# Optimization experiments

Hardware: AMD Instinct MI355X
Metric: run time of the kernel (lower is better)

The kernel has to match this reference:

```python
import jax, jax.numpy as jnp
import numpy as np

B, D, L = 16384, 4096, 6


def setup_inputs() -> dict:
    key = jax.random.key(0)
    k_x, k_w = jax.random.split(key)
    inputs = jax.random.normal(k_x, (B, D), dtype=jnp.float32)
    # xavier_uniform for each [D, 1] slice: bound = sqrt(6 / (D + 1))
    bound = float(np.sqrt(6.0 / (D + 1)))
    w = jax.random.uniform(k_w, (L, D, 1), dtype=jnp.float32, minval=-bound, maxval=bound)
    b = jnp.zeros((L, D), dtype=jnp.float32)
    return {"inputs": inputs, "w": w, "b": b}


def reference(inputs, w, b):
    # DCN cross layers: x_{i+1} = x0 * (x @ w_i) + b_i + x
    x0 = inputs  # [B, D]

    def step(x, wb):
        wi, bi = wb                      # wi: [D, 1], bi: [D]
        xw = jnp.matmul(x, wi)           # [B, 1] matvec
        x_new = x0 * xw + bi + x         # fused elementwise mul + bias + residual
        return x_new, None

    x, _ = jax.lax.scan(step, inputs, (w, b))
    # use_bn=False, dropout=0 -> output is x
    return x
```

## Files before the change

kernel.cpp:

```cpp
#include <hip/hip_runtime.h>


#define BATCH 16384
#define DIM   4096
#define NLAYER 6
#define BLK 256
#define VPT 4

__global__ __launch_bounds__(BLK) void crossnet_kernel(
    const float* __restrict__ xin,
    const float* __restrict__ w,
    const float* __restrict__ bias,
    float* __restrict__ out)
{
    const int row  = blockIdx.x;
    const int tid  = threadIdx.x;
    const int lane = tid & 63;
    const int wave = tid >> 6;

    const float4* xrow = (const float4*)(xin + (size_t)row * DIM);

    float4 x0v[VPT], xv[VPT];
#pragma unroll
    for (int j = 0; j < VPT; ++j) {
        x0v[j] = xrow[tid + j * BLK];
        xv[j]  = x0v[j];
    }

    __shared__ float red[2][4];

    for (int l = 0; l < NLAYER; ++l) {
        const float4* wl = (const float4*)(w + l * DIM);
        float p = 0.0f;
#pragma unroll
        for (int j = 0; j < VPT; ++j) {
            float4 wv = wl[tid + j * BLK];
            p = fmaf(xv[j].x, wv.x, p);
            p = fmaf(xv[j].y, wv.y, p);
            p = fmaf(xv[j].z, wv.z, p);
            p = fmaf(xv[j].w, wv.w, p);
        }
#pragma unroll
        for (int off = 32; off > 0; off >>= 1)
            p += __shfl_down(p, off, 64);
        if (lane == 0) red[l & 1][wave] = p;
        __syncthreads();
        const float s = red[l & 1][0] + red[l & 1][1] + red[l & 1][2] + red[l & 1][3];

        const float4* bl = (const float4*)(bias + l * DIM);
#pragma unroll
        for (int j = 0; j < VPT; ++j) {
            float4 bv = bl[tid + j * BLK];
            xv[j].x = fmaf(x0v[j].x, s, bv.x + xv[j].x);
            xv[j].y = fmaf(x0v[j].y, s, bv.y + xv[j].y);
            xv[j].z = fmaf(x0v[j].z, s, bv.z + xv[j].z);
            xv[j].w = fmaf(x0v[j].w, s, bv.w + xv[j].w);
        }
    }

    float4* orow = (float4*)(out + (size_t)row * DIM);
#pragma unroll
    for (int j = 0; j < VPT; ++j)
        orow[tid + j * BLK] = xv[j];
}

extern "C" void kernel_launch(void* const* d_in, const int* in_sizes, int n_in,
                              void* d_out, int out_size, void* d_ws, size_t ws_size,
                              hipStream_t stream) {
    const float* xin  = (const float*)d_in[0];
    const float* w    = (const float*)d_in[1];
    const float* bias = (const float*)d_in[2];
    float* out = (float*)d_out;

    crossnet_kernel<<<BATCH, BLK, 0, stream>>>(xin, w, bias, out);
}
```

Measured before the change: 506.5 us.

## Collapse cross layers into one row scale plus a precomputed bias vector

Uses the fact that every layer's state can be written as a_l*x0 + c_l, where a_l is a per-row scalar and c_l is a running sum of biases. The six per-layer dot products x0·w_l are computed together with a single reduction and one barrier. The final row is then formed as a*x0 + c in one pass. A small single-block kernel precomputes c and the scalars c_l·w_l, which adds a launch and a dependency ahead of the main kernel. Floating-point summation order changes.

New measurement: 503.9 us. No clear change (-0.5%).

```diff
diff --git a/kernel.cpp b/kernel.cpp
--- a/kernel.cpp
+++ b/kernel.cpp
@@ -1,16 +1,62 @@
 #include <hip/hip_runtime.h>
 
 
-#define BATCH 16384
-#define DIM   4096
+#define BATCH  16384
+#define DIM    4096
 #define NLAYER 6
-#define BLK 256
-#define VPT 4
+#define BLK    256
+#define VPT    4
+
+__global__ __launch_bounds__(1024) void precompute_kernel(
+    const float* __restrict__ w,
+    const float* __restrict__ bias,
+    float* __restrict__ c_out,
+    float* __restrict__ d_out)
+{
+    const int tid  = threadIdx.x;
+    const int lane = tid & 63;
+    const int wave = tid >> 6;
+
+    float dpart[NLAYER];
+#pragma unroll
+    for (int l = 0; l < NLAYER; ++l) dpart[l] = 0.0f;
+
+#pragma unroll
+    for (int k = 0; k < DIM / 1024; ++k) {
+        const int j = tid + k * 1024;
+        float pre = 0.0f;
+#pragma unroll
+        for (int l = 0; l < NLAYER; ++l) {
+            dpart[l] = fmaf(pre, w[l * DIM + j], dpart[l]);
+            pre += bias[l * DIM + j];
+        }
+        c_out[j] = pre;
+    }
+
+#pragma unroll
+    for (int l = 0; l < NLAYER; ++l)
+#pragma unroll
+        for (int off = 32; off > 0; off >>= 1)
+            dpart[l] += __shfl_xor(dpart[l], off, 64);
+
+    __shared__ float red[16][NLAYER];
+    if (lane == 0)
+#pragma unroll
+        for (int l = 0; l < NLAYER; ++l) red[wave][l] = dpart[l];
+    __syncthreads();
+    if (tid < NLAYER) {
+        float s = 0.0f;
+#pragma unroll
+        for (int wv = 0; wv < 16; ++wv) s += red[wv][tid];
+        d_out[tid] = s;
+    }
+}
 
 __global__ __launch_bounds__(BLK) void crossnet_kernel(
     const float* __restrict__ xin,
     const float* __restrict__ w,
-    const float* __restrict__ bias,
+    const float* __restrict__ c,
+    const float* __restrict__ d,
     float* __restrict__ out)
 {
     const int row  = blockIdx.x;
@@ -20,48 +66,58 @@
 
     const float4* xrow = (const float4*)(xin + (size_t)row * DIM);
 
-    float4 x0v[VPT], xv[VPT];
+    float4 x0v[VPT];
 #pragma unroll
-    for (int j = 0; j < VPT; ++j) {
+    for (int j = 0; j < VPT; ++j)
         x0v[j] = xrow[tid + j * BLK];
-        xv[j]  = x0v[j];
-    }
 
-    __shared__ float red[2][4];
-
+    float u[NLAYER];
+#pragma unroll
+    for (int l = 0; l < NLAYER; ++l) u[l] = 0.0f;
+#pragma unroll
     for (int l = 0; l < NLAYER; ++l) {
         const float4* wl = (const float4*)(w + l * DIM);
-        float p = 0.0f;
 #pragma unroll
         for (int j = 0; j < VPT; ++j) {
             float4 wv = wl[tid + j * BLK];
-            p = fmaf(xv[j].x, wv.x, p);
-            p = fmaf(xv[j].y, wv.y, p);
-            p = fmaf(xv[j].z, wv.z, p);
-            p = fmaf(xv[j].w, wv.w, p);
-        }
-#pragma unroll
-        for (int off = 32; off > 0; off >>= 1)
-            p += __shfl_down(p, off, 64);
-        if (lane == 0) red[l & 1][wave] = p;
-        __syncthreads();
-        const float s = red[l & 1][0] + red[l & 1][1] + red[l & 1][2] + red[l & 1][3];
-
-        const float4* bl = (const float4*)(bias + l * DIM);
-#pragma unroll
-        for (int j = 0; j < VPT; ++j) {
-            float4 bv = bl[tid + j * BLK];
-            xv[j].x = fmaf(x0v[j].x, s, bv.x + xv[j].x);
-            xv[j].y = fmaf(x0v[j].y, s, bv.y + xv[j].y);
-            xv[j].z = fmaf(x0v[j].z, s, bv.z + xv[j].z);
-            xv[j].w = fmaf(x0v[j].w, s, bv.w + xv[j].w);
+            u[l] = fmaf(x0v[j].x, wv.x, u[l]);
+            u[l] = fmaf(x0v[j].y, wv.y, u[l]);
+            u[l] = fmaf(x0v[j].z, wv.z, u[l]);
+            u[l] = fmaf(x0v[j].w, wv.w, u[l]);
         }
     }
 
-    float4* orow = (float4*)(out + (size_t)row * DIM);
 #pragma unroll
-    for (int j = 0; j < VPT; ++j)
-        orow[tid + j * BLK] = xv[j];
+    for (int l = 0; l < NLAYER; ++l)
+#pragma unroll
+        for (int off = 32; off > 0; off >>= 1)
+            u[l] += __shfl_xor(u[l], off, 64);
+
+    __shared__ float red[4][NLAYER];
+    if (lane == 0)
+#pragma unroll
+        for (int l = 0; l < NLAYER; ++l) red[wave][l] = u[l];
+    __syncthreads();
+
+    float a = 1.0f;
+#pragma unroll
+    for (int l = 0; l < NLAYER; ++l) {
+        const float s = red[0][l] + red[1][l] + red[2][l] + red[3][l];
+        a = fmaf(a, s, a) + d[l];
+    }
+
+    const float4* cr   = (const float4*)c;
+    float4*       orow = (float4*)(out + (size_t)row * DIM);
+#pragma unroll
+    for (int j = 0; j < VPT; ++j) {
+        float4 cv = cr[tid + j * BLK];
+        float4 o;
+        o.x = fmaf(x0v[j].x, a, cv.x);
+        o.y = fmaf(x0v[j].y, a, cv.y);
+        o.z = fmaf(x0v[j].z, a, cv.z);
+        o.w = fmaf(x0v[j].w, a, cv.w);
+        orow[tid + j * BLK] = o;
+    }
 }
 
 extern "C" void kernel_launch(void* const* d_in, const int* in_sizes, int n_in,
@@ -72,5 +128,9 @@
     const float* bias = (const float*)d_in[2];
     float* out = (float*)d_out;
 
-    crossnet_kernel<<<BATCH, BLK, 0, stream>>>(xin, w, bias, out);
+    float* c = (float*)d_ws;
+    float* d = c + DIM;
+
+    precompute_kernel<<<1, 1024, 0, stream>>>(w, bias, c, d);
+    crossnet_kernel<<<BATCH, BLK, 0, stream>>>(xin, w, c, d, out);
 }
```
